# Performance work log

Hardware: AMD Instinct MI355X
Metric: run time of the kernel (lower is better)

## Reference

```python
import jax, jax.numpy as jnp
import numpy as np

B, IN_SEQ, HID_SEQ, OUT_SEQ = 2, 2048, 2048, 2048
C_IN, C_OUT, H = 1024, 1024, 16
HD = C_OUT // H  # 64


def _linear_params(key, out_f, in_f):
    kw, kb = jax.random.split(key)
    bound = 1.0 / np.sqrt(in_f)
    w = jax.random.uniform(kw, (out_f, in_f), jnp.float32, -bound, bound)
    b = jax.random.uniform(kb, (out_f,), jnp.float32, -bound, bound)
    return w, b


def setup_inputs() -> dict:
    key = jax.random.key(0)
    ks = jax.random.split(key, 6)
    x = jax.random.normal(ks[0], (B, IN_SEQ, C_IN), jnp.float32)
    w_hseq, b_hseq = _linear_params(ks[1], HID_SEQ, IN_SEQ)
    wq, bq = _linear_params(ks[2], C_OUT, C_IN)
    wk, bk = _linear_params(ks[3], C_OUT, C_IN)
    wv, bv = _linear_params(ks[4], C_OUT, C_IN)
    w_oseq, b_oseq = _linear_params(ks[5], OUT_SEQ, HID_SEQ)
    return {"x": x, "w_hseq": w_hseq, "b_hseq": b_hseq,
            "wq": wq, "bq": bq, "wk": wk, "bk": bk, "wv": wv, "bv": bv,
            "w_oseq": w_oseq, "b_oseq": b_oseq}


def reference(x, w_hseq, b_hseq, wq, bq, wk, bk, wv, bv, w_oseq, b_oseq):
    b = x.shape[0]
    # seq-axis projection: Linear(in_seq -> hidden_seq) applied to x.transpose(1,2)
    # xh[b, t, c] = sum_s x[b, s, c] * w_hseq[t, s] + b_hseq[t]
    xh = jnp.einsum('bsc,ts->btc', x, w_hseq) + b_hseq[:, None]
    q = (xh @ wq.T + bq).reshape(b, HID_SEQ, H, HD).transpose(0, 2, 1, 3)  # [B,H,Sh,hd]
    k = (xh @ wk.T + bk).reshape(b, HID_SEQ, H, HD).transpose(0, 2, 1, 3)
    v = (xh @ wv.T + bv).reshape(b, HID_SEQ, H, HD).transpose(0, 2, 1, 3)
    scores = jnp.einsum('bhqd,bhkd->bhqk', q, k) / np.sqrt(HD).astype(np.float32)
    attn = jax.nn.softmax(scores, axis=-1)                       # [B,H,Sh,Sh]
    flex = jnp.einsum('bhqk,ok->bhqo', attn, w_oseq) + b_oseq    # [B,H,Sh,So]
    # flexscale.transpose(-2,-1) @ v contracts over the QUERY axis q
    out = jnp.einsum('bhqo,bhqd->bhod', flex, v)                 # [B,H,So,hd]
    return out.transpose(0, 2, 1, 3).reshape(b, OUT_SEQ, C_OUT)
```

## Files before the change

### kernel.cpp

```cpp
#include <hip/hip_runtime.h>
#include <hip/hip_bf16.h>

typedef unsigned short u16;
typedef unsigned int u32;
typedef unsigned long long u64;
typedef __attribute__((ext_vector_type(8))) short s16x8;
typedef __attribute__((ext_vector_type(4))) float f32x4;
typedef __attribute__((ext_vector_type(16))) float f32x16;

#define SCL 0.1803368867f

#if __has_builtin(__builtin_amdgcn_exp2f)
#define EXP2(x) __builtin_amdgcn_exp2f(x)
#else
#define EXP2(x) exp2f(x)
#endif

__device__ __forceinline__ float bf2f(u16 v){ u32 u = ((u32)v)<<16; return __builtin_bit_cast(float,u); }
__device__ __forceinline__ u16 f2bf(float f){
  u32 u = __builtin_bit_cast(u32,f);
  u += 0x7fff + ((u>>16)&1);
  return (u16)(u>>16);
}
__device__ __forceinline__ u32 pkbf(float a, float b){
  u32 ua = __builtin_bit_cast(u32,a) + 0x8000u;
  u32 ub = __builtin_bit_cast(u32,b) + 0x8000u;
  return (ua>>16) | (ub & 0xFFFF0000u);
}
__device__ __forceinline__ void glds16(const u16* g, const u16* lds_u){
  __builtin_amdgcn_global_load_lds(
      (const __attribute__((address_space(1))) void*)(u64)g,
      (__attribute__((address_space(3))) void*)(u32)(u64)lds_u,
      16, 0, 0);
}
__device__ __forceinline__ f32x4 mfma16(s16x8 a, s16x8 b, f32x4 c){
  return __builtin_amdgcn_mfma_f32_16x16x32_bf16(a,b,c,0,0,0);
}
__device__ __forceinline__ f32x16 mfma32(s16x8 a, s16x8 b, f32x16 c){
  return __builtin_amdgcn_mfma_f32_32x32x16_bf16(a,b,c,0,0,0);
}

__global__ __launch_bounds__(256) void detect_dtype(const u16* __restrict__ x, u32* __restrict__ flag){
  __shared__ int cnt;
  if (threadIdx.x==0) cnt = 0;
  __syncthreads();
  int local = 0;
  for (int i = threadIdx.x; i < 4096; i += 256){
    u16 v = x[2*i];
    int e = (v>>7)&0xFF;
    if (e >= 140 || e <= 100) local++;
  }
  atomicAdd(&cnt, local);
  __syncthreads();
  if (threadIdx.x==0) *flag = (cnt > 1024) ? 1u : 0u;
}

struct CvtArgs { const void* src[10]; u16* dst[10]; int n[10]; };

__global__ __launch_bounds__(256) void convert_inputs(CvtArgs a, const u32* __restrict__ flag){
  const int which = blockIdx.y;
  const int n = a.n[which];
  const int base = blockIdx.x*2048 + threadIdx.x;
  if (base >= n) return;
  u16* dst = a.dst[which];
  if (*flag){
    const float* s = (const float*)a.src[which];
    #pragma unroll
    for (int j=0;j<8;j++){ int i = base + j*256; if (i<n) dst[i] = f2bf(s[i]); }
  } else {
    const u16* s = (const u16*)a.src[which];
    #pragma unroll
    for (int j=0;j<8;j++){ int i = base + j*256; if (i<n) dst[i] = s[i]; }
  }
}

__global__ __launch_bounds__(256) void transpose_x(
    const void* __restrict__ src, const u32* __restrict__ flag, u16* __restrict__ dst)
{
  __shared__ u16 T[64][72];
  const int s0 = blockIdx.x*64, c0 = blockIdx.y*64, b = blockIdx.z;
  const int t = threadIdx.x;
  const int r = t>>2, cc = (t&3)*16;
  const long off = ((long)(b*2048 + s0 + r))*1024 + c0 + cc;
  if (*flag){
    const float* p = (const float*)src + off;
    #pragma unroll
    for (int j=0;j<16;j++) T[r][cc+j] = f2bf(p[j]);
  } else {
    const u16* p = (const u16*)src + off;
    *(s16x8*)&T[r][cc]   = *(const s16x8*)p;
    *(s16x8*)&T[r][cc+8] = *(const s16x8*)(p+8);
  }
  __syncthreads();
  {
    const int orow = t&63, oc = (t>>6)*16;
    u16 tmp[16];
    #pragma unroll
    for (int j=0;j<16;j++) tmp[j] = T[oc+j][orow];
    u16* q = dst + (long)b*2097152 + (long)(c0+orow)*2048 + s0 + oc;
    *(s16x8*)q     = *(s16x8*)&tmp[0];
    *(s16x8*)(q+8) = *(s16x8*)&tmp[8];
  }
}

__global__ __launch_bounds__(256) void transpose_scale_k(
    const u16* __restrict__ qkv, const float* __restrict__ lS, u16* __restrict__ dst)
{
  __shared__ u16 T[64][72];
  __shared__ float ils[64];
  const int s0 = blockIdx.x*64, c0 = blockIdx.y*64, b = blockIdx.z;
  const int t = threadIdx.x;
  if (t < 64) ils[t] = lS[((long)(b*16 + (c0>>6)))*2048 + s0 + t];
  __syncthreads();
  {
    const int r = t>>2, cc = (t&3)*16;
    const u16* p = qkv + (long)b*6291456 + (long)(s0+r)*3072 + 2048 + c0 + cc;
    const float sc = ils[r];
    s16x8 v0 = *(const s16x8*)p, v1 = *(const s16x8*)(p+8);
    #pragma unroll
    for (int j=0;j<8;j++){
      T[r][cc+j]   = f2bf(bf2f((u16)v0[j])*sc);
      T[r][cc+8+j] = f2bf(bf2f((u16)v1[j])*sc);
    }
  }
  __syncthreads();
  {
    const int orow = t&63, oc = (t>>6)*16;
    u16 tmp[16];
    #pragma unroll
    for (int j=0;j<16;j++) tmp[j] = T[oc+j][orow];
    u16* q = dst + (long)b*2097152 + (long)(c0+orow)*2048 + s0 + oc;
    *(s16x8*)q     = *(s16x8*)&tmp[0];
    *(s16x8*)(q+8) = *(s16x8*)&tmp[8];
  }
}

__global__ __launch_bounds__(256) void rowsum_part(const u16* __restrict__ qkv, float* __restrict__ svp){
  const int c = blockIdx.x*256 + threadIdx.x;
  const int b = c>>10, cc = c&1023;
  const int tz = blockIdx.y;
  const u16* p = qkv + ((long)(b*2048 + tz*256))*3072 + 2048 + cc;
  float s = 0.f;
  #pragma unroll 8
  for (int i=0;i<256;i++) s += bf2f(p[(long)i*3072]);
  svp[tz*2048 + c] = s;
}
__global__ __launch_bounds__(256) void rowsum_fin(const float* __restrict__ svp, float* __restrict__ sv){
  const int c = blockIdx.x*256 + threadIdx.x;
  float s = 0.f;
  #pragma unroll
  for (int z=0;z<8;z++) s += svp[z*2048 + c];
  sv[c] = s;
}

template<int BN, int BMODE, bool DYN, bool QS>
__global__ __launch_bounds__(256) void gemm_t(
    const u16* __restrict__ A, const u16* __restrict__ B,
    const u16* __restrict__ bias, const float* __restrict__ r1col,
    const u32* __restrict__ dflag, void* __restrict__ C,
    int K, int lda, int ldb, int ldc,
    long aBatch, long bBatch, long cBatch)
{
  constexpr int BM = 128;
  constexpr int ACH = BM/64, BCH = BN/64;
  constexpr int MI = (BN==128) ? 4 : 2;
  __shared__ u16 As[2][BM*32];
  __shared__ u16 Bs[2][BN*32];
  const int t = threadIdx.x, w = t>>6, quad = (t&63)>>4, l16 = t&15;
  const int z = blockIdx.z;
  const int m0 = blockIdx.x*BM, n0 = blockIdx.y*BN;
  const u16* Ag = A + (long)z*aBatch + (long)m0*lda;
  const u16* Bg = B + (long)z*bBatch + (long)n0*ldb;
  const int wm = (BN==128) ? (w>>1)*64 : w*32;
  const int wn = (BN==128) ? (w&1)*64 : 0;

  auto stage = [&](int buf, int k0){
    #pragma unroll
    for (int i=0;i<ACH;i++){
      const int chunk = i*256 + t;
      glds16(Ag + (long)(chunk>>2)*lda + k0 + (chunk&3)*8, &As[buf][(i*256 + w*64)*8]);
    }
    #pragma unroll
    for (int i=0;i<BCH;i++){
      const int chunk = i*256 + t;
      glds16(Bg + (long)(chunk>>2)*ldb + k0 + (chunk&3)*8, &Bs[buf][(i*256 + w*64)*8]);
    }
  };

  f32x4 acc[MI][4];
  #pragma unroll
  for (int i=0;i<MI;i++)
    #pragma unroll
    for (int j=0;j<4;j++) acc[i][j] = (f32x4){0.f,0.f,0.f,0.f};

  stage(0, 0);
  const int nk = K>>5;
  for (int kt=0; kt<nk; ++kt){
    __syncthreads();
    if (kt+1 < nk) stage((kt+1)&1, (kt+1)<<5);
    const u16* as = As[kt&1];
    const u16* bs = Bs[kt&1];
    s16x8 a[MI], bb[4];
    #pragma unroll
    for (int i=0;i<MI;i++) a[i] = *(const s16x8*)&as[(wm + i*16 + l16)*32 + quad*8];
    #pragma unroll
    for (int j=0;j<4;j++)  bb[j]= *(const s16x8*)&bs[(wn + j*16 + l16)*32 + quad*8];
    #pragma unroll
    for (int i=0;i<MI;i++)
      #pragma unroll
      for (int j=0;j<4;j++)
        acc[i][j] = mfma16(a[i], bb[j], acc[i][j]);
  }

  bool f32o = false;
  if (DYN) f32o = (*dflag != 0);
  #pragma unroll
  for (int i=0;i<MI;i++){
    #pragma unroll
    for (int j=0;j<4;j++){
      const int col = n0 + wn + j*16 + l16;
      #pragma unroll
      for (int r=0;r<4;r++){
        const int row = m0 + wm + i*16 + quad*4 + r;
        float vv = acc[i][j][r];
        if (BMODE==1) vv += bf2f(bias[row]);
        if (BMODE==2) vv += bf2f(bias[col]);
        if (BMODE==3) vv += bf2f(bias[row]) * r1col[z*1024 + col];
        if (QS){ if (col < 1024) vv *= SCL; }
        const long idx = (long)z*cBatch + (long)row*ldc + col;
        if (DYN && f32o) ((float*)C)[idx] = vv;
        else             ((u16*)C)[idx]   = f2bf(vv);
      }
    }
  }
}

__global__ __launch_bounds__(256) void attn_stats(const u16* __restrict__ qkv, float* __restrict__ lS){
  __shared__ u16 Qs[64][68];
  __shared__ u16 Ks[64][68];
  __shared__ float red[2][64];
  const int q0 = blockIdx.x*64, bh = blockIdx.y, b = bh>>4, h = bh&15;
  const int t = threadIdx.x, w = t>>6, l32 = t&31, half = (t&63)>>5;
  const int wq = w>>1, wk = w&1;
  {
    const int r = t>>2, cc = (t&3)*16;
    const u16* p = &qkv[((long)(b*2048 + q0 + r))*3072 + h*64 + cc];
    *(s16x8*)&Qs[r][cc]   = *(const s16x8*)p;
    *(s16x8*)&Qs[r][cc+8] = *(const s16x8*)(p+8);
  }
  __syncthreads();
  s16x8 aq[4];
  #pragma unroll
  for (int u=0;u<4;u++) aq[u] = *(s16x8*)&Qs[wq*32 + l32][u*16 + half*8];
  float lp[16];
  #pragma unroll
  for (int r=0;r<16;r++) lp[r] = 0.f;

  for (int kc=0; kc<2048; kc+=64){
    __syncthreads();
    {
      const int r = t>>2, cc = (t&3)*16;
      const u16* p = &qkv[((long)(b*2048 + kc + r))*3072 + 1024 + h*64 + cc];
      *(s16x8*)&Ks[r][cc]   = *(const s16x8*)p;
      *(s16x8*)&Ks[r][cc+8] = *(const s16x8*)(p+8);
    }
    __syncthreads();
    s16x8 kb[4];
    #pragma unroll
    for (int u=0;u<4;u++) kb[u] = *(s16x8*)&Ks[wk*32 + l32][u*16 + half*8];
    f32x16 acc = {};
    #pragma unroll
    for (int u=0;u<4;u++) acc = mfma32(aq[u], kb[u], acc);
    #pragma unroll
    for (int r=0;r<16;r++) lp[r] += EXP2(acc[r]);
  }
  #pragma unroll
  for (int off=1; off<32; off<<=1)
    #pragma unroll
    for (int r=0;r<16;r++) lp[r] += __shfl_xor(lp[r], off);
  if (l32 == 0){
    #pragma unroll
    for (int r=0;r<16;r++)
      red[wk][wq*32 + 4*half + (r&3) + 8*(r>>2)] = lp[r];
  }
  __syncthreads();
  if (t < 64){
    float l = red[0][t] + red[1][t];
    lS[(long)bh*2048 + q0 + t] = 1.f/l;
  }
}

__global__ __launch_bounds__(256) void attn_pv(
    const u16* __restrict__ qkv, const u16* __restrict__ VtG, u16* __restrict__ Mt)
{
  __shared__ u16 Ks[64][68];
  __shared__ u16 Qs[64][68];
  __shared__ u16 Vs[64][68];
  __shared__ u16 Ps[64][68];
  const int k0 = blockIdx.x*64, bh = blockIdx.y, b = bh>>4, h = bh&15;
  const int t = threadIdx.x, w = t>>6, l32 = t&31, half = (t&63)>>5;
  const int wr = w>>1, wk = w&1;
  {
    const int r = t>>2, cc = (t&3)*16;
    const u16* p = &qkv[((long)(b*2048 + k0 + r))*3072 + 1024 + h*64 + cc];
    *(s16x8*)&Ks[r][cc]   = *(const s16x8*)p;
    *(s16x8*)&Ks[r][cc+8] = *(const s16x8*)(p+8);
  }
  __syncthreads();
  s16x8 kb[4];
  #pragma unroll
  for (int u=0;u<4;u++) kb[u] = *(s16x8*)&Ks[wk*32 + l32][u*16 + half*8];

  f32x16 accM = {};
  for (int q0=0; q0<2048; q0+=64){
    __syncthreads();
    {
      const int r = t>>2, cc = (t&3)*16;
      const u16* pq = &qkv[((long)(b*2048 + q0 + r))*3072 + h*64 + cc];
      *(s16x8*)&Qs[r][cc]   = *(const s16x8*)pq;
      *(s16x8*)&Qs[r][cc+8] = *(const s16x8*)(pq+8);
      const u16* pv = &VtG[((long)(b*1024 + h*64 + r))*2048 + q0 + cc];
      *(s16x8*)&Vs[r][cc]   = *(const s16x8*)pv;
      *(s16x8*)&Vs[r][cc+8] = *(const s16x8*)(pv+8);
    }
    __syncthreads();
    s16x8 aq[4];
    #pragma unroll
    for (int u=0;u<4;u++) aq[u] = *(s16x8*)&Qs[wr*32 + l32][u*16 + half*8];
    f32x16 acc = {};
    #pragma unroll
    for (int u=0;u<4;u++) acc = mfma32(aq[u], kb[u], acc);
    const int kcol = wk*32 + l32;
    #pragma unroll
    for (int g=0; g<4; g++){
      float p0 = EXP2(acc[4*g+0]);
      float p1 = EXP2(acc[4*g+1]);
      float p2 = EXP2(acc[4*g+2]);
      float p3 = EXP2(acc[4*g+3]);
      u64 v = (u64)pkbf(p0,p1) | ((u64)pkbf(p2,p3) << 32);
      *(u64*)&Ps[kcol][wr*32 + 8*g + 4*half] = v;
    }
    __syncthreads();
    s16x8 av[4], bp[4];
    #pragma unroll
    for (int u=0;u<4;u++) av[u] = *(s16x8*)&Vs[wr*32 + l32][u*16 + half*8];
    #pragma unroll
    for (int u=0;u<4;u++) bp[u] = *(s16x8*)&Ps[wk*32 + l32][u*16 + half*8];
    #pragma unroll
    for (int u=0;u<4;u++) accM = mfma32(av[u], bp[u], accM);
  }
  #pragma unroll
  for (int r=0;r<16;r++){
    const int d = wr*32 + 4*half + (r&3) + 8*(r>>2);
    const int k = k0 + wk*32 + l32;
    Mt[((long)(b*1024 + h*64 + d))*2048 + k] = f2bf(accM[r]);
  }
}

extern "C" void kernel_launch(void* const* d_in, const int* in_sizes, int n_in,
                              void* d_out, int out_size, void* d_ws, size_t ws_size,
                              hipStream_t stream)
{
  (void)n_in; (void)out_size; (void)ws_size;
  char* ws = (char*)d_ws;
  u32*  dflag = (u32*)ws;            ws += 64;
  u16*  whc   = (u16*)ws;            ws += (size_t)8388608;
  u16*  wqkvc = (u16*)ws;            ws += (size_t)6291456;
  u16*  woc   = (u16*)ws;            ws += (size_t)8388608;
  u16*  bhc   = (u16*)ws;            ws += 4096;
  u16*  bqkvc = (u16*)ws;            ws += 8192;
  u16*  boc   = (u16*)ws;            ws += 4096;
  u16*  xT    = (u16*)ws;            ws += (size_t)8388608;
  u16*  xh    = (u16*)ws;            ws += (size_t)8388608;
  u16*  qkvb  = (u16*)ws;            ws += (size_t)25165824;
  u16*  VtG   = (u16*)ws;            ws += (size_t)8388608;
  u16*  Mt    = (u16*)ws;            ws += (size_t)8388608;
  float* lS   = (float*)ws;          ws += (size_t)262144;
  float* svp  = (float*)ws;          ws += (size_t)65536;
  float* sv   = (float*)ws;          ws += 8192;

  detect_dtype<<<1,256,0,stream>>>((const u16*)d_in[0], dflag);
  CvtArgs ca;
  const void* srcs[10] = {d_in[1], d_in[2], d_in[3], d_in[4], d_in[5],
                          d_in[6], d_in[7], d_in[8], d_in[9], d_in[10]};
  u16* dsts[10] = {whc, bhc, wqkvc, bqkvc, wqkvc+1048576, bqkvc+1024,
                   wqkvc+2097152, bqkvc+2048, woc, boc};
  const int ns[10] = {in_sizes[1], in_sizes[2], in_sizes[3], in_sizes[4], in_sizes[5],
                      in_sizes[6], in_sizes[7], in_sizes[8], in_sizes[9], in_sizes[10]};
  for (int i=0;i<10;i++){ ca.src[i]=srcs[i]; ca.dst[i]=dsts[i]; ca.n[i]=ns[i]; }
  convert_inputs<<<dim3(2048,10),256,0,stream>>>(ca, dflag);

  const long S2M = 2097152L;

  transpose_x<<<dim3(32,16,2),256,0,stream>>>(d_in[0], dflag, xT);

  gemm_t<64,1,false,false><<<dim3(16,16,2),256,0,stream>>>(whc, xT, bhc, nullptr, dflag, xh,
      2048, 2048, 2048, 1024, 0L, S2M, S2M);

  gemm_t<128,2,false,true><<<dim3(16,24,2),256,0,stream>>>(xh, wqkvc, bqkvc, nullptr, dflag, qkvb,
      1024, 1024, 1024, 3072, S2M, 0L, (long)2048*3072);

  rowsum_part<<<dim3(8,8),256,0,stream>>>(qkvb, svp);
  rowsum_fin<<<8,256,0,stream>>>(svp, sv);

  attn_stats<<<dim3(32,32),256,0,stream>>>(qkvb, lS);

  transpose_scale_k<<<dim3(32,16,2),256,0,stream>>>(qkvb, lS, VtG);

  attn_pv<<<dim3(32,32),256,0,stream>>>(qkvb, VtG, Mt);

  gemm_t<64,3,true,false><<<dim3(16,16,2),256,0,stream>>>(woc, Mt, boc, sv, dflag, d_out,
      2048, 2048, 2048, 1024, 0L, S2M, S2M);
}
```

Baseline: 353.9 us.

## Double-buffer P/V tiles in attn_pv and enlarge GEMM tiles for seq projections

In attn_pv, the P and V shared tiles are double-buffered so each iteration's PV MFMA on the previous tile runs after the single barrier. This removes one __syncthreads per iteration and lets the PV product overlap with the next QK tile. Separately, the two seq-axis GEMMs switch from 64 to 128 tile height with half as many blocks along y, trading occupancy and grid size for more data reuse. The double buffers add extra LDS use per block.

```diff
diff --git a/kernel.cpp b/kernel.cpp
--- a/kernel.cpp
+++ b/kernel.cpp
@@ -295,16 +295,16 @@
 {
   __shared__ u16 Ks[64][68];
   __shared__ u16 Qs[64][68];
-  __shared__ u16 Vs[64][68];
-  __shared__ u16 Ps[64][68];
+  __shared__ u16 Vs[2][64][68];
+  __shared__ u16 Ps[2][64][68];
   const int k0 = blockIdx.x*64, bh = blockIdx.y, b = bh>>4, h = bh&15;
   const int t = threadIdx.x, w = t>>6, l32 = t&31, half = (t&63)>>5;
   const int wr = w>>1, wk = w&1;
-  {
-    const int r = t>>2, cc = (t&3)*16;
-    const u16* p = &qkv[((long)(b*2048 + k0 + r))*3072 + 1024 + h*64 + cc];
-    *(s16x8*)&Ks[r][cc]   = *(const s16x8*)p;
-    *(s16x8*)&Ks[r][cc+8] = *(const s16x8*)(p+8);
+  const int sr = t>>2, scc = (t&3)*16;
+  {
+    const u16* p = &qkv[((long)(b*2048 + k0 + sr))*3072 + 1024 + h*64 + scc];
+    *(s16x8*)&Ks[sr][scc]   = *(const s16x8*)p;
+    *(s16x8*)&Ks[sr][scc+8] = *(const s16x8*)(p+8);
   }
   __syncthreads();
   s16x8 kb[4];
@@ -312,18 +312,27 @@
   for (int u=0;u<4;u++) kb[u] = *(s16x8*)&Ks[wk*32 + l32][u*16 + half*8];
 
   f32x16 accM = {};
-  for (int q0=0; q0<2048; q0+=64){
+  for (int i=0; i<32; i++){
+    const int q0 = i*64;
     __syncthreads();
     {
-      const int r = t>>2, cc = (t&3)*16;
-      const u16* pq = &qkv[((long)(b*2048 + q0 + r))*3072 + h*64 + cc];
-      *(s16x8*)&Qs[r][cc]   = *(const s16x8*)pq;
-      *(s16x8*)&Qs[r][cc+8] = *(const s16x8*)(pq+8);
-      const u16* pv = &VtG[((long)(b*1024 + h*64 + r))*2048 + q0 + cc];
-      *(s16x8*)&Vs[r][cc]   = *(const s16x8*)pv;
-      *(s16x8*)&Vs[r][cc+8] = *(const s16x8*)(pv+8);
+      const u16* pq = &qkv[((long)(b*2048 + q0 + sr))*3072 + h*64 + scc];
+      *(s16x8*)&Qs[sr][scc]   = *(const s16x8*)pq;
+      *(s16x8*)&Qs[sr][scc+8] = *(const s16x8*)(pq+8);
+      const u16* pv = &VtG[((long)(b*1024 + h*64 + sr))*2048 + q0 + scc];
+      *(s16x8*)&Vs[i&1][sr][scc]   = *(const s16x8*)pv;
+      *(s16x8*)&Vs[i&1][sr][scc+8] = *(const s16x8*)(pv+8);
     }
     __syncthreads();
+    if (i > 0){
+      s16x8 av[4], bp[4];
+      #pragma unroll
+      for (int u=0;u<4;u++) av[u] = *(s16x8*)&Vs[(i-1)&1][wr*32 + l32][u*16 + half*8];
+      #pragma unroll
+      for (int u=0;u<4;u++) bp[u] = *(s16x8*)&Ps[(i-1)&1][wk*32 + l32][u*16 + half*8];
+      #pragma unroll
+      for (int u=0;u<4;u++) accM = mfma32(av[u], bp[u], accM);
+    }
     s16x8 aq[4];
     #pragma unroll
     for (int u=0;u<4;u++) aq[u] = *(s16x8*)&Qs[wr*32 + l32][u*16 + half*8];
@@ -338,14 +347,16 @@
       float p2 = EXP2(acc[4*g+2]);
       float p3 = EXP2(acc[4*g+3]);
       u64 v = (u64)pkbf(p0,p1) | ((u64)pkbf(p2,p3) << 32);
-      *(u64*)&Ps[kcol][wr*32 + 8*g + 4*half] = v;
-    }
-    __syncthreads();
+      *(u64*)&Ps[i&1][kcol][wr*32 + 8*g + 4*half] = v;
+    }
+  }
+  __syncthreads();
+  {
     s16x8 av[4], bp[4];
     #pragma unroll
-    for (int u=0;u<4;u++) av[u] = *(s16x8*)&Vs[wr*32 + l32][u*16 + half*8];
-    #pragma unroll
-    for (int u=0;u<4;u++) bp[u] = *(s16x8*)&Ps[wk*32 + l32][u*16 + half*8];
+    for (int u=0;u<4;u++) av[u] = *(s16x8*)&Vs[1][wr*32 + l32][u*16 + half*8];
+    #pragma unroll
+    for (int u=0;u<4;u++) bp[u] = *(s16x8*)&Ps[1][wk*32 + l32][u*16 + half*8];
     #pragma unroll
     for (int u=0;u<4;u++) accM = mfma32(av[u], bp[u], accM);
   }
@@ -394,7 +405,7 @@
 
   transpose_x<<<dim3(32,16,2),256,0,stream>>>(d_in[0], dflag, xT);
 
-  gemm_t<64,1,false,false><<<dim3(16,16,2),256,0,stream>>>(whc, xT, bhc, nullptr, dflag, xh,
+  gemm_t<128,1,false,false><<<dim3(16,8,2),256,0,stream>>>(whc, xT, bhc, nullptr, dflag, xh,
       2048, 2048, 2048, 1024, 0L, S2M, S2M);
 
   gemm_t<128,2,false,true><<<dim3(16,24,2),256,0,stream>>>(xh, wqkvc, bqkvc, nullptr, dflag, qkvb,
@@ -409,6 +420,6 @@
 
   attn_pv<<<dim3(32,32),256,0,stream>>>(qkvb, VtG, Mt);
 
-  gemm_t<64,3,true,false><<<dim3(16,16,2),256,0,stream>>>(woc, Mt, boc, sv, dflag, d_out,
+  gemm_t<128,3,true,false><<<dim3(16,8,2),256,0,stream>>>(woc, Mt, boc, sv, dflag, d_out,
       2048, 2048, 2048, 1024, 0L, S2M, S2M);
 }
```

After: 371.4 us. +4.9%, slower.
